# Performance work log

Hardware: AMD Instinct MI355X
Metric: run time of the kernel (lower is better)

Reference implementation:

```python
import jax, jax.numpy as jnp
import numpy as np

B, S, HIDDEN = 4, 2048, 1024
NUM_EXPERTS = 8
TOP_K = 4
EPS = 1e-6


def setup_inputs() -> dict:
    key = jax.random.key(0)
    k0, k1, k2 = jax.random.split(key, 3)
    x = jax.random.normal(k0, (B, S, HIDDEN), dtype=jnp.float32)
    Wg = jax.random.normal(k1, (HIDDEN, NUM_EXPERTS), dtype=jnp.float32) * 0.02
    bg = jnp.zeros((NUM_EXPERTS,), dtype=jnp.float32)
    W = jax.random.normal(k2, (NUM_EXPERTS, HIDDEN, HIDDEN), dtype=jnp.float32) * 0.02
    b = jnp.zeros((NUM_EXPERTS, HIDDEN), dtype=jnp.float32)
    return {"x": x, "Wg": Wg, "bg": bg, "W": W, "b": b}


def reference(x, Wg, bg, W, b):
    Bb, Ss, D = x.shape
    xf = x.reshape(-1, D)                       # [T, D]
    T = xf.shape[0]

    # --- router ---
    router_logits = xf @ Wg + bg                # [T, E]
    router_probs = jax.nn.softmax(router_logits, axis=-1)
    top_k_probs, top_k_indices = jax.lax.top_k(router_probs, TOP_K)  # [T, K]
    top_k_weights = top_k_probs / (top_k_probs.sum(axis=-1, keepdims=True) + EPS)
    expert_mask = jax.nn.one_hot(top_k_indices, NUM_EXPERTS, dtype=jnp.float32).sum(axis=1)  # [T, E]

    # --- experts: original computes every expert on every token then masks;
    # same math expressed as one batched GEMM + gather ---
    all_out = jnp.einsum('td,edf->etf', xf, W) + b[:, None, :]  # [E, T, D]
    sel = all_out[top_k_indices.T, jnp.arange(T)[None, :]]      # [K, T, D]
    moe_output = jnp.einsum('tk,ktd->td', top_k_weights, sel).reshape(Bb, Ss, D)

    # --- load-balancing aux loss ---
    aux_loss = jnp.dot(expert_mask.mean(axis=0), router_probs.mean(axis=0)) * NUM_EXPERTS
    return moe_output, aux_loss
```

## Files before the change

kernel.cpp:

```cpp
#include <hip/hip_runtime.h>
#include <hip/hip_bf16.h>

#define T_TOK 8192
#define DH    1024
#define NE    8
#define TK    4

typedef unsigned short u16;
typedef __bf16 bf16x8 __attribute__((ext_vector_type(8)));
typedef float  f32x4  __attribute__((ext_vector_type(4)));

__device__ __forceinline__ u16 f2b(float f) {
    union { float f; unsigned u; } v; v.f = f;
    unsigned u = v.u;
    u += 0x7FFFu + ((u >> 16) & 1u);
    return (u16)(u >> 16);
}
__device__ __forceinline__ float b2f(u16 h) {
    union { unsigned u; float f; } v; v.u = ((unsigned)h) << 16;
    return v.f;
}
__device__ __forceinline__ void glds16(const u16* g, u16* l) {
    __builtin_amdgcn_global_load_lds((const __attribute__((address_space(1))) void*)g,
                                     (__attribute__((address_space(3))) void*)l, 16, 0, 0);
}

__global__ __launch_bounds__(256) void cast_w_kernel(const float* __restrict__ W,
                                                     u16* __restrict__ wbt) {
    __shared__ float tile[64][65];
    const int e  = blockIdx.z;
    const int d0 = blockIdx.y * 64;
    const int f0 = blockIdx.x * 64;
    const int r  = threadIdx.x >> 4;
    const int c4 = (threadIdx.x & 15) * 4;
    const float* src = W + ((size_t)e << 20) + (size_t)d0 * DH + f0;
    #pragma unroll
    for (int i = 0; i < 4; i++) {
        const int row = i * 16 + r;
        const float4 v = *(const float4*)(src + (size_t)row * DH + c4);
        tile[row][c4]     = v.x;
        tile[row][c4 + 1] = v.y;
        tile[row][c4 + 2] = v.z;
        tile[row][c4 + 3] = v.w;
    }
    __syncthreads();
    u16* dst = wbt + ((size_t)e << 20) + (size_t)f0 * DH + d0;
    #pragma unroll
    for (int i = 0; i < 4; i++) {
        const int orow = i * 16 + r;
        ushort4 o;
        o.x = f2b(tile[c4][orow]);
        o.y = f2b(tile[c4 + 1][orow]);
        o.z = f2b(tile[c4 + 2][orow]);
        o.w = f2b(tile[c4 + 3][orow]);
        *(ushort4*)(dst + (size_t)orow * DH + c4) = o;
    }
}

__global__ __launch_bounds__(512) void router_kernel(
    const float* __restrict__ x, const float* __restrict__ Wg, const float* __restrict__ bg,
    u16* __restrict__ xb,
    int* __restrict__ bucket_tok, float* __restrict__ bucket_w,
    int* __restrict__ tk_e, float* __restrict__ tk_w,
    int* __restrict__ cnt, float* __restrict__ probsum)
{
    __shared__ int   lcnt[NE];
    __shared__ float lprob[NE];
    __shared__ int   gbase[NE];
    const int tid = threadIdx.x;
    const int wv = tid >> 6, lane = tid & 63;
    const int t = blockIdx.x * 8 + wv;
    if (tid < NE) { lcnt[tid] = 0; lprob[tid] = 0.f; }
    __syncthreads();

    float a[NE] = {};
    {
        const float* xr = x + (size_t)t * DH;
        u16* xbr = xb + (size_t)t * DH;
        #pragma unroll
        for (int it = 0; it < 4; it++) {
            const int d = it * 256 + lane * 4;
            const float4 v = *(const float4*)(xr + d);
            ushort4 o;
            o.x = f2b(v.x); o.y = f2b(v.y); o.z = f2b(v.z); o.w = f2b(v.w);
            *(ushort4*)(xbr + d) = o;
            const float* wr = Wg + d * NE;
            #pragma unroll
            for (int e = 0; e < NE; e++)
                a[e] += v.x * wr[e] + v.y * wr[NE + e] + v.z * wr[2 * NE + e] + v.w * wr[3 * NE + e];
        }
    }
    #pragma unroll
    for (int e = 0; e < NE; e++) {
        float v = a[e];
        #pragma unroll
        for (int off = 32; off > 0; off >>= 1) v += __shfl_down(v, off);
        a[e] = v;
    }

    int idx4[TK]; float w4[TK]; int off4[TK];
    if (lane == 0) {
        float logits[NE], probs[NE];
        float mx = -1e30f;
        #pragma unroll
        for (int e = 0; e < NE; e++) { logits[e] = a[e] + bg[e]; mx = fmaxf(mx, logits[e]); }
        float Z = 0.f;
        #pragma unroll
        for (int e = 0; e < NE; e++) { probs[e] = expf(logits[e] - mx); Z += probs[e]; }
        const float rZ = 1.f / Z;
        #pragma unroll
        for (int e = 0; e < NE; e++) probs[e] *= rZ;

        float rem2[NE];
        #pragma unroll
        for (int e = 0; e < NE; e++) rem2[e] = probs[e];
        float s4 = 0.f;
        #pragma unroll
        for (int k = 0; k < TK; k++) {
            int best = 0; float bv = rem2[0];
            #pragma unroll
            for (int e = 1; e < NE; e++) if (rem2[e] > bv) { bv = rem2[e]; best = e; }
            idx4[k] = best; w4[k] = bv; s4 += bv; rem2[best] = -1e30f;
        }
        const float rs = 1.f / (s4 + 1e-6f);
        #pragma unroll
        for (int k = 0; k < TK; k++) {
            w4[k] *= rs;
            tk_e[t * TK + k] = idx4[k];
            tk_w[t * TK + k] = w4[k];
            off4[k] = atomicAdd(&lcnt[idx4[k]], 1);
        }
        #pragma unroll
        for (int e = 0; e < NE; e++) atomicAdd(&lprob[e], probs[e]);
    }
    __syncthreads();
    if (tid < NE) {
        gbase[tid] = atomicAdd(&cnt[tid], lcnt[tid]);
        atomicAdd(&probsum[tid], lprob[tid]);
    }
    __syncthreads();
    if (lane == 0) {
        #pragma unroll
        for (int k = 0; k < TK; k++) {
            const int e = idx4[k];
            const int slot = gbase[e] + off4[k];
            bucket_tok[e * T_TOK + slot] = (t << 2) | k;
            bucket_w[e * T_TOK + slot]   = w4[k];
        }
    }
}

__global__ __launch_bounds__(256) void moe_gemm_kernel(
    const u16* __restrict__ xb, const u16* __restrict__ wbt,
    const int* __restrict__ bucket_tok, const float* __restrict__ bucket_w,
    const int* __restrict__ cnt, u16* __restrict__ y)
{
    const int e  = blockIdx.z;
    const int M  = cnt[e];
    const int m0 = blockIdx.y * 128;
    if (m0 >= M) return;
    const int n0 = blockIdx.x * 128;

    __shared__ u16 As[128 * 32];
    __shared__ u16 Bs[128 * 32];
    __shared__ int   s_tok[128];
    __shared__ float s_w[128];

    const int tid  = threadIdx.x;
    const int lane = tid & 63;
    const int wave = tid >> 6;

    if (tid < 128) {
        const int slot = m0 + tid;
        if (slot < M) {
            s_tok[tid] = bucket_tok[e * T_TOK + slot];
            s_w[tid]   = bucket_w[e * T_TOK + slot];
        } else { s_tok[tid] = -1; s_w[tid] = 0.f; }
    }
    __syncthreads();

    const int l4 = lane >> 2;
    const int c8 = (lane & 3) * 8;
    const int r0 = (2 * wave) * 16 + l4;
    const int r1 = r0 + 16;
    const int t0 = s_tok[r0], t1 = s_tok[r1];
    const u16* gA0 = xb + (size_t)(t0 >= 0 ? (t0 >> 2) : 0) * DH + c8;
    const u16* gA1 = xb + (size_t)(t1 >= 0 ? (t1 >> 2) : 0) * DH + c8;
    const u16* gB0 = wbt + ((size_t)e << 20) + (size_t)(n0 + r0) * DH + c8;
    const u16* gB1 = gB0 + (size_t)16 * DH;
    u16* lA0 = &As[(2 * wave)     * 512];
    u16* lA1 = &As[(2 * wave + 1) * 512];
    u16* lB0 = &Bs[(2 * wave)     * 512];
    u16* lB1 = &Bs[(2 * wave + 1) * 512];

    const int mrow = (wave >> 1) * 64;
    const int ncol = (wave & 1) * 64;
    const int fr   = lane & 15;
    const int fq   = (lane >> 4) * 8;

    f32x4 acc[4][4] = {};

    for (int k0 = 0; k0 < DH; k0 += 32) {
        glds16(gA0 + k0, lA0);
        glds16(gA1 + k0, lA1);
        glds16(gB0 + k0, lB0);
        glds16(gB1 + k0, lB1);
        __syncthreads();
        bf16x8 af[4], bfv[4];
        #pragma unroll
        for (int i = 0; i < 4; i++)
            af[i] = *(const bf16x8*)&As[(mrow + i * 16 + fr) * 32 + fq];
        #pragma unroll
        for (int j = 0; j < 4; j++)
            bfv[j] = *(const bf16x8*)&Bs[(ncol + j * 16 + fr) * 32 + fq];
        #pragma unroll
        for (int i = 0; i < 4; i++)
            #pragma unroll
            for (int j = 0; j < 4; j++)
                acc[i][j] = __builtin_amdgcn_mfma_f32_16x16x32_bf16(af[i], bfv[j], acc[i][j], 0, 0, 0);
        __syncthreads();
    }

    const int cl = lane & 15;
    const int rb = (lane >> 4) * 4;
    #pragma unroll
    for (int i = 0; i < 4; i++) {
        #pragma unroll
        for (int r = 0; r < 4; r++) {
            const int srow = mrow + i * 16 + rb + r;
            const int tok = s_tok[srow];
            if (tok < 0) continue;
            const float w = s_w[srow];
            u16* yr = y + (size_t)tok * DH + (n0 + ncol + cl);
            #pragma unroll
            for (int j = 0; j < 4; j++)
                yr[j * 16] = f2b(acc[i][j][r] * w);
        }
    }
}

__global__ __launch_bounds__(256) void combine_kernel(
    const u16* __restrict__ y, const int* __restrict__ tk_e, const float* __restrict__ tk_w,
    const float* __restrict__ bexp,
    const int* __restrict__ cnt, const float* __restrict__ probsum,
    float* __restrict__ out, float* __restrict__ out_aux)
{
    const int t = blockIdx.x;
    const int c = threadIdx.x * 4;
    if (t == 0 && threadIdx.x == 0) {
        float s = 0.f;
        for (int e = 0; e < NE; e++) s += (float)cnt[e] * probsum[e];
        out_aux[0] = s * (float)NE / ((float)T_TOK * (float)T_TOK);
    }
    float o0 = 0.f, o1 = 0.f, o2 = 0.f, o3 = 0.f;
    #pragma unroll
    for (int k = 0; k < TK; k++) {
        const int e   = tk_e[t * TK + k];
        const float w = tk_w[t * TK + k];
        const ushort4 yv = *(const ushort4*)(y + ((size_t)(t * TK + k)) * DH + c);
        const float4  bv = *(const float4*)(bexp + (size_t)e * DH + c);
        o0 += b2f(yv.x) + w * bv.x;
        o1 += b2f(yv.y) + w * bv.y;
        o2 += b2f(yv.z) + w * bv.z;
        o3 += b2f(yv.w) + w * bv.w;
    }
    float4 ov = {o0, o1, o2, o3};
    *(float4*)(out + (size_t)t * DH + c) = ov;
}

extern "C" void kernel_launch(void* const* d_in, const int* in_sizes, int n_in,
                              void* d_out, int out_size, void* d_ws, size_t ws_size,
                              hipStream_t stream)
{
    const float* x  = (const float*)d_in[0];
    const float* Wg = (const float*)d_in[1];
    const float* bg = (const float*)d_in[2];
    const float* W  = (const float*)d_in[3];
    const float* b  = (const float*)d_in[4];
    float* out = (float*)d_out;

    char* ws = (char*)d_ws;
    u16*   xb         = (u16*)(ws);
    u16*   wbt        = (u16*)(ws + 16777216);
    u16*   y          = (u16*)(ws + 33554432);
    int*   bucket_tok = (int*)(ws + 100663296);
    float* bucket_w   = (float*)(ws + 100925440);
    int*   tk_e       = (int*)(ws + 101187584);
    float* tk_w       = (float*)(ws + 101318656);
    int*   cnt        = (int*)(ws + 101449728);
    float* probsum    = (float*)(ws + 101449760);

    hipMemsetAsync(cnt, 0, 64, stream);

    cast_w_kernel<<<dim3(16, 16, NE), 256, 0, stream>>>(W, wbt);
    router_kernel<<<1024, 512, 0, stream>>>(x, Wg, bg, xb, bucket_tok, bucket_w, tk_e, tk_w, cnt, probsum);
    moe_gemm_kernel<<<dim3(8, 64, NE), 256, 0, stream>>>(xb, wbt, bucket_tok, bucket_w, cnt, y);
    combine_kernel<<<8192, 256, 0, stream>>>(y, tk_e, tk_w, b, cnt, probsum, out, out + (size_t)T_TOK * DH);
}
```

Before: 257.5 us.

## Enlarge expert GEMM tile to 256x128 with 64x128 per-wave subtiles

Doubles the M dimension of the per-block tile in the grouped expert GEMM to 256 tokens and reorganizes the four waves so each computes a 64x128 output strip (4x8 MFMA accumulators). This raises arithmetic intensity per LDS load and halves redundant weight-tile reloads across M blocks. The cost is twice the accumulator registers, which may lower occupancy or spill, and fewer blocks in a grid that is already partly idle because of per-expert token imbalance.

```diff
diff --git a/kernel.cpp b/kernel.cpp
--- a/kernel.cpp
+++ b/kernel.cpp
@@ -157,20 +157,20 @@
 {
     const int e  = blockIdx.z;
     const int M  = cnt[e];
-    const int m0 = blockIdx.y * 128;
+    const int m0 = blockIdx.y * 256;
     if (m0 >= M) return;
     const int n0 = blockIdx.x * 128;
 
-    __shared__ u16 As[128 * 32];
+    __shared__ u16 As[256 * 32];
     __shared__ u16 Bs[128 * 32];
-    __shared__ int   s_tok[128];
-    __shared__ float s_w[128];
+    __shared__ int   s_tok[256];
+    __shared__ float s_w[256];
 
     const int tid  = threadIdx.x;
     const int lane = tid & 63;
     const int wave = tid >> 6;
 
-    if (tid < 128) {
+    {
         const int slot = m0 + tid;
         if (slot < M) {
             s_tok[tid] = bucket_tok[e * T_TOK + slot];
@@ -181,42 +181,47 @@
 
     const int l4 = lane >> 2;
     const int c8 = (lane & 3) * 8;
-    const int r0 = (2 * wave) * 16 + l4;
-    const int r1 = r0 + 16;
-    const int t0 = s_tok[r0], t1 = s_tok[r1];
-    const u16* gA0 = xb + (size_t)(t0 >= 0 ? (t0 >> 2) : 0) * DH + c8;
-    const u16* gA1 = xb + (size_t)(t1 >= 0 ? (t1 >> 2) : 0) * DH + c8;
-    const u16* gB0 = wbt + ((size_t)e << 20) + (size_t)(n0 + r0) * DH + c8;
-    const u16* gB1 = gB0 + (size_t)16 * DH;
-    u16* lA0 = &As[(2 * wave)     * 512];
-    u16* lA1 = &As[(2 * wave + 1) * 512];
-    u16* lB0 = &Bs[(2 * wave)     * 512];
-    u16* lB1 = &Bs[(2 * wave + 1) * 512];
-
-    const int mrow = (wave >> 1) * 64;
-    const int ncol = (wave & 1) * 64;
+    const u16* wb_e = wbt + ((size_t)e << 20);
+    const u16* gA[4]; u16* lA[4];
+    const u16* gB[2]; u16* lB[2];
+    #pragma unroll
+    for (int j = 0; j < 4; j++) {
+        const int seg = wave * 4 + j;
+        const int row = seg * 16 + l4;
+        const int tj  = s_tok[row];
+        gA[j] = xb + (size_t)(tj >= 0 ? (tj >> 2) : 0) * DH + c8;
+        lA[j] = &As[seg * 512];
+    }
+    #pragma unroll
+    for (int j = 0; j < 2; j++) {
+        const int seg = wave * 2 + j;
+        gB[j] = wb_e + (size_t)(n0 + seg * 16 + l4) * DH + c8;
+        lB[j] = &Bs[seg * 512];
+    }
+
+    const int mrow = wave * 64;
     const int fr   = lane & 15;
     const int fq   = (lane >> 4) * 8;
 
-    f32x4 acc[4][4] = {};
+    f32x4 acc[4][8] = {};
 
     for (int k0 = 0; k0 < DH; k0 += 32) {
-        glds16(gA0 + k0, lA0);
-        glds16(gA1 + k0, lA1);
-        glds16(gB0 + k0, lB0);
-        glds16(gB1 + k0, lB1);
+        #pragma unroll
+        for (int j = 0; j < 4; j++) glds16(gA[j] + k0, lA[j]);
+        #pragma unroll
+        for (int j = 0; j < 2; j++) glds16(gB[j] + k0, lB[j]);
         __syncthreads();
-        bf16x8 af[4], bfv[4];
+        bf16x8 af[4], bfv[8];
         #pragma unroll
         for (int i = 0; i < 4; i++)
             af[i] = *(const bf16x8*)&As[(mrow + i * 16 + fr) * 32 + fq];
         #pragma unroll
-        for (int j = 0; j < 4; j++)
-            bfv[j] = *(const bf16x8*)&Bs[(ncol + j * 16 + fr) * 32 + fq];
+        for (int j = 0; j < 8; j++)
+            bfv[j] = *(const bf16x8*)&Bs[(j * 16 + fr) * 32 + fq];
         #pragma unroll
         for (int i = 0; i < 4; i++)
             #pragma unroll
-            for (int j = 0; j < 4; j++)
+            for (int j = 0; j < 8; j++)
                 acc[i][j] = __builtin_amdgcn_mfma_f32_16x16x32_bf16(af[i], bfv[j], acc[i][j], 0, 0, 0);
         __syncthreads();
     }
@@ -231,9 +236,9 @@
             const int tok = s_tok[srow];
             if (tok < 0) continue;
             const float w = s_w[srow];
-            u16* yr = y + (size_t)tok * DH + (n0 + ncol + cl);
+            u16* yr = y + (size_t)tok * DH + (n0 + cl);
             #pragma unroll
-            for (int j = 0; j < 4; j++)
+            for (int j = 0; j < 8; j++)
                 yr[j * 16] = f2b(acc[i][j][r] * w);
         }
     }
@@ -294,6 +299,6 @@
 
     cast_w_kernel<<<dim3(16, 16, NE), 256, 0, stream>>>(W, wbt);
     router_kernel<<<1024, 512, 0, stream>>>(x, Wg, bg, xb, bucket_tok, bucket_w, tk_e, tk_w, cnt, probsum);
-    moe_gemm_kernel<<<dim3(8, 64, NE), 256, 0, stream>>>(xb, wbt, bucket_tok, bucket_w, cnt, y);
+    moe_gemm_kernel<<<dim3(8, 32, NE), 256, 0, stream>>>(xb, wbt, bucket_tok, bucket_w, cnt, y);
     combine_kernel<<<8192, 256, 0, stream>>>(y, tk_e, tk_w, b, cnt, probsum, out, out + (size_t)T_TOK * DH);
 }
```

Result: slower. 330.3 us (+28.3%).

## Fuse combine into GEMM epilogue via fp32 atomics, init output with bias in router

Applied to the files above, without the earlier changes.

Removes the separate combine kernel and the bf16 intermediate y buffer. The router now writes each token's weighted bias sum straight into the output. The GEMM epilogue then atomically adds its weighted fp32 partial results into that output, and the aux-loss computation moves into the GEMM kernel. This cuts a kernel launch and a large round trip through global memory, but it adds scattered fp32 atomic adds (four experts per element) and makes the summation order nondeterministic.

```diff
diff --git a/kernel.cpp b/kernel.cpp
--- a/kernel.cpp
+++ b/kernel.cpp
@@ -15,10 +15,6 @@
     unsigned u = v.u;
     u += 0x7FFFu + ((u >> 16) & 1u);
     return (u16)(u >> 16);
-}
-__device__ __forceinline__ float b2f(u16 h) {
-    union { unsigned u; float f; } v; v.u = ((unsigned)h) << 16;
-    return v.f;
 }
 __device__ __forceinline__ void glds16(const u16* g, u16* l) {
     __builtin_amdgcn_global_load_lds((const __attribute__((address_space(1))) void*)g,
@@ -59,14 +55,16 @@
 
 __global__ __launch_bounds__(512) void router_kernel(
     const float* __restrict__ x, const float* __restrict__ Wg, const float* __restrict__ bg,
-    u16* __restrict__ xb,
+    const float* __restrict__ bexp,
+    u16* __restrict__ xb, float* __restrict__ out,
     int* __restrict__ bucket_tok, float* __restrict__ bucket_w,
-    int* __restrict__ tk_e, float* __restrict__ tk_w,
     int* __restrict__ cnt, float* __restrict__ probsum)
 {
     __shared__ int   lcnt[NE];
     __shared__ float lprob[NE];
     __shared__ int   gbase[NE];
+    __shared__ int   s_sel[8][TK];
+    __shared__ float s_sw[8][TK];
     const int tid = threadIdx.x;
     const int wv = tid >> 6, lane = tid & 63;
     const int t = blockIdx.x * 8 + wv;
@@ -126,8 +124,8 @@
         #pragma unroll
         for (int k = 0; k < TK; k++) {
             w4[k] *= rs;
-            tk_e[t * TK + k] = idx4[k];
-            tk_w[t * TK + k] = w4[k];
+            s_sel[wv][k] = idx4[k];
+            s_sw[wv][k]  = w4[k];
             off4[k] = atomicAdd(&lcnt[idx4[k]], 1);
         }
         #pragma unroll
@@ -148,14 +146,42 @@
             bucket_w[e * T_TOK + slot]   = w4[k];
         }
     }
+    {
+        const float* b0 = bexp + (size_t)s_sel[wv][0] * DH;
+        const float* b1 = bexp + (size_t)s_sel[wv][1] * DH;
+        const float* b2 = bexp + (size_t)s_sel[wv][2] * DH;
+        const float* b3 = bexp + (size_t)s_sel[wv][3] * DH;
+        const float w0 = s_sw[wv][0], w1 = s_sw[wv][1], w2 = s_sw[wv][2], w3 = s_sw[wv][3];
+        float* orow = out + (size_t)t * DH;
+        #pragma unroll
+        for (int it = 0; it < 4; it++) {
+            const int d = it * 256 + lane * 4;
+            const float4 v0 = *(const float4*)(b0 + d);
+            const float4 v1 = *(const float4*)(b1 + d);
+            const float4 v2 = *(const float4*)(b2 + d);
+            const float4 v3 = *(const float4*)(b3 + d);
+            float4 o;
+            o.x = w0 * v0.x + w1 * v1.x + w2 * v2.x + w3 * v3.x;
+            o.y = w0 * v0.y + w1 * v1.y + w2 * v2.y + w3 * v3.y;
+            o.z = w0 * v0.z + w1 * v1.z + w2 * v2.z + w3 * v3.z;
+            o.w = w0 * v0.w + w1 * v1.w + w2 * v2.w + w3 * v3.w;
+            *(float4*)(orow + d) = o;
+        }
+    }
 }
 
 __global__ __launch_bounds__(256) void moe_gemm_kernel(
     const u16* __restrict__ xb, const u16* __restrict__ wbt,
     const int* __restrict__ bucket_tok, const float* __restrict__ bucket_w,
-    const int* __restrict__ cnt, u16* __restrict__ y)
+    const int* __restrict__ cnt, const float* __restrict__ probsum,
+    float* __restrict__ out, float* __restrict__ out_aux)
 {
     const int e  = blockIdx.z;
+    if (e == 0 && blockIdx.x == 0 && blockIdx.y == 0 && threadIdx.x == 0) {
+        float s = 0.f;
+        for (int i = 0; i < NE; i++) s += (float)cnt[i] * probsum[i];
+        out_aux[0] = s * (float)NE / ((float)T_TOK * (float)T_TOK);
+    }
     const int M  = cnt[e];
     const int m0 = blockIdx.y * 128;
     if (m0 >= M) return;
@@ -231,41 +257,12 @@
             const int tok = s_tok[srow];
             if (tok < 0) continue;
             const float w = s_w[srow];
-            u16* yr = y + (size_t)tok * DH + (n0 + ncol + cl);
+            float* orow = out + (size_t)(tok >> 2) * DH + (n0 + ncol + cl);
             #pragma unroll
             for (int j = 0; j < 4; j++)
-                yr[j * 16] = f2b(acc[i][j][r] * w);
-        }
-    }
-}
-
-__global__ __launch_bounds__(256) void combine_kernel(
-    const u16* __restrict__ y, const int* __restrict__ tk_e, const float* __restrict__ tk_w,
-    const float* __restrict__ bexp,
-    const int* __restrict__ cnt, const float* __restrict__ probsum,
-    float* __restrict__ out, float* __restrict__ out_aux)
-{
-    const int t = blockIdx.x;
-    const int c = threadIdx.x * 4;
-    if (t == 0 && threadIdx.x == 0) {
-        float s = 0.f;
-        for (int e = 0; e < NE; e++) s += (float)cnt[e] * probsum[e];
-        out_aux[0] = s * (float)NE / ((float)T_TOK * (float)T_TOK);
-    }
-    float o0 = 0.f, o1 = 0.f, o2 = 0.f, o3 = 0.f;
-    #pragma unroll
-    for (int k = 0; k < TK; k++) {
-        const int e   = tk_e[t * TK + k];
-        const float w = tk_w[t * TK + k];
-        const ushort4 yv = *(const ushort4*)(y + ((size_t)(t * TK + k)) * DH + c);
-        const float4  bv = *(const float4*)(bexp + (size_t)e * DH + c);
-        o0 += b2f(yv.x) + w * bv.x;
-        o1 += b2f(yv.y) + w * bv.y;
-        o2 += b2f(yv.z) + w * bv.z;
-        o3 += b2f(yv.w) + w * bv.w;
-    }
-    float4 ov = {o0, o1, o2, o3};
-    *(float4*)(out + (size_t)t * DH + c) = ov;
+                atomicAdd(orow + j * 16, acc[i][j][r] * w);
+        }
+    }
 }
 
 extern "C" void kernel_launch(void* const* d_in, const int* in_sizes, int n_in,
@@ -282,18 +279,16 @@
     char* ws = (char*)d_ws;
     u16*   xb         = (u16*)(ws);
     u16*   wbt        = (u16*)(ws + 16777216);
-    u16*   y          = (u16*)(ws + 33554432);
-    int*   bucket_tok = (int*)(ws + 100663296);
-    float* bucket_w   = (float*)(ws + 100925440);
-    int*   tk_e       = (int*)(ws + 101187584);
-    float* tk_w       = (float*)(ws + 101318656);
-    int*   cnt        = (int*)(ws + 101449728);
-    float* probsum    = (float*)(ws + 101449760);
+    int*   bucket_tok = (int*)(ws + 33554432);
+    float* bucket_w   = (float*)(ws + 33816576);
+    int*   cnt        = (int*)(ws + 34078720);
+    float* probsum    = (float*)(ws + 34078752);
 
     hipMemsetAsync(cnt, 0, 64, stream);
 
     cast_w_kernel<<<dim3(16, 16, NE), 256, 0, stream>>>(W, wbt);
-    router_kernel<<<1024, 512, 0, stream>>>(x, Wg, bg, xb, bucket_tok, bucket_w, tk_e, tk_w, cnt, probsum);
-    moe_gemm_kernel<<<dim3(8, 64, NE), 256, 0, stream>>>(xb, wbt, bucket_tok, bucket_w, cnt, y);
-    combine_kernel<<<8192, 256, 0, stream>>>(y, tk_e, tk_w, b, cnt, probsum, out, out + (size_t)T_TOK * DH);
-}
+    router_kernel<<<1024, 512, 0, stream>>>(x, Wg, bg, b, xb, out,
+                                            bucket_tok, bucket_w, cnt, probsum);
+    moe_gemm_kernel<<<dim3(8, 64, NE), 256, 0, stream>>>(xb, wbt, bucket_tok, bucket_w,
+                                                         cnt, probsum, out, out + (size_t)T_TOK * DH);
+}
```

New measurement: 314.8 us. +22.3%, slower.
